# Kernel optimization log

Hardware: AMD Instinct MI355X
Metric: run time of the kernel (lower is better)

## Reference

```python
import jax, jax.numpy as jnp
import numpy as np

DIM = 1024
NUM_HEADS = 16
WINDOW_SIZE = 512
HEAD_DIM = DIM // NUM_HEADS
SCALE = HEAD_DIM ** (-0.5)


def setup_inputs() -> dict:
    key = jax.random.key(0)
    kq, kk, kv = jax.random.split(key, 3)
    shape = (2, NUM_HEADS, 2048, HEAD_DIM)
    q = jax.random.normal(kq, shape, dtype=jnp.float32)
    k = jax.random.normal(kk, shape, dtype=jnp.float32)
    v = jax.random.normal(kv, shape, dtype=jnp.float32)
    return {"q": q, "k": k, "v": v}


def reference(q, k, v):
    B, H, N, D = q.shape
    pos = jnp.arange(N)
    # causal + sliding window: col <= row and col >= row - w + 1
    window_mask = (pos[None, :] <= pos[:, None]) & (pos[None, :] >= pos[:, None] - WINDOW_SIZE + 1)  # (N, N)
    attn = jnp.einsum("bhnd,bhmd->bhnm", q, k) * SCALE  # (B, H, N, N)
    attn = jnp.where(window_mask[None, None], attn, -jnp.inf)
    attn = jax.nn.softmax(attn, axis=-1)
    attn = jnp.nan_to_num(attn, nan=0.0)
    return jnp.einsum("bhnm,bhmd->bhnd", attn, v)
```

## Files before the change

kernel.cpp:

```cpp
#include <hip/hip_runtime.h>
#include <math.h>


#define SEQ 2048
#define HD  64
#define BM  64
#define BN  64
#define LDR 72

typedef short short8 __attribute__((ext_vector_type(8)));
typedef float f32x4  __attribute__((ext_vector_type(4)));

static __device__ inline unsigned short f2bf(float f){
  union{float f; unsigned u;} un; un.f=f;
  return (unsigned short)((un.u + 0x7FFFu + ((un.u>>16)&1u))>>16);
}

__global__ __launch_bounds__(256) void swa_fwd(
    const float* __restrict__ q, const float* __restrict__ k,
    const float* __restrict__ v, float* __restrict__ out)
{
  __shared__ short Qs[BM*LDR];
  __shared__ short Ps[BM*LDR];
  __shared__ short Ks[2][BN*LDR];
  __shared__ short Vt[2][HD*LDR];

  const int tid=threadIdx.x, bid=blockIdx.x;
  const int mtile=bid&31, bh=bid>>5, m0=mtile*BM;
  const long base=(long)bh*SEQ*HD;
  const int wv=tid>>6, lane=tid&63, quad=lane>>4, l16=lane&15;
  const int dcol=lane;

  {
    const float4* qg=(const float4*)(q+base+(long)m0*HD);
    #pragma unroll
    for(int i=0;i<4;++i){
      int idx=i*256+tid, r=idx>>4, c4=idx&15;
      float4 f=qg[idx];
      ushort4 h; h.x=f2bf(f.x); h.y=f2bf(f.y); h.z=f2bf(f.z); h.w=f2bf(f.w);
      *(ushort4*)&Qs[r*LDR+c4*4]=h;
    }
  }

  const int tb=mtile, tlo=(tb>8)?(tb-8):0;

  float4 kreg[4];
  float  vcol[4][4];
  {
    const float4* kg=(const float4*)(k+base+(long)(tlo*BN)*HD);
    const float*  vg=v+base+(long)(tlo*BN)*HD;
    #pragma unroll
    for(int i=0;i<4;++i) kreg[i]=kg[i*256+tid];
    #pragma unroll
    for(int g=0;g<4;++g){
      int r0=wv*4+g*16;
      #pragma unroll
      for(int j=0;j<4;++j) vcol[g][j]=vg[(r0+j)*HD+dcol];
    }
  }
  __syncthreads();

  short8 qa[2];
  #pragma unroll
  for(int kk=0;kk<2;++kk)
    qa[kk]=*(const short8*)&Qs[(wv*16+l16)*LDR+kk*32+quad*8];

  {
    #pragma unroll
    for(int i=0;i<4;++i){
      int idx=i*256+tid, r=idx>>4, c4=idx&15;
      float4 fk=kreg[i];
      ushort4 hk; hk.x=f2bf(fk.x); hk.y=f2bf(fk.y); hk.z=f2bf(fk.z); hk.w=f2bf(fk.w);
      *(ushort4*)&Ks[0][r*LDR+c4*4]=hk;
    }
    #pragma unroll
    for(int g=0;g<4;++g){
      int r0=wv*4+g*16;
      ushort4 hv; hv.x=f2bf(vcol[g][0]); hv.y=f2bf(vcol[g][1]);
                  hv.z=f2bf(vcol[g][2]); hv.w=f2bf(vcol[g][3]);
      *(ushort4*)&Vt[0][dcol*LDR+r0]=hv;
    }
  }

  float lrun[4]={0.f,0.f,0.f,0.f};
  f32x4 oacc[4];
  #pragma unroll
  for(int dt=0;dt<4;++dt) oacc[dt]=(f32x4){0.f,0.f,0.f,0.f};

  __syncthreads();

  for(int t=tlo;t<=tb;++t){
    const int buf=(t-tlo)&1;
    const int j0=t*BN;

    f32x4 sacc[4];
    #pragma unroll
    for(int nt=0;nt<4;++nt) sacc[nt]=(f32x4){0.f,0.f,0.f,0.f};
    #pragma unroll
    for(int kk=0;kk<2;++kk){
      #pragma unroll
      for(int nt=0;nt<4;++nt){
        short8 kb=*(const short8*)&Ks[buf][(nt*16+l16)*LDR+kk*32+quad*8];
        sacc[nt]=__builtin_amdgcn_mfma_f32_16x16x32_bf16(qa[kk],kb,sacc[nt],0,0,0);
      }
    }

    if(t<tb){
      const float4* kg=(const float4*)(k+base+(long)((t+1)*BN)*HD);
      const float*  vg=v+base+(long)((t+1)*BN)*HD;
      #pragma unroll
      for(int i=0;i<4;++i) kreg[i]=kg[i*256+tid];
      #pragma unroll
      for(int g=0;g<4;++g){
        int r0=wv*4+g*16;
        #pragma unroll
        for(int j=0;j<4;++j) vcol[g][j]=vg[(r0+j)*HD+dcol];
      }
    }

    #pragma unroll
    for(int r=0;r<4;++r){
      const int grr=m0+wv*16+quad*4+r;
      #pragma unroll
      for(int nt=0;nt<4;++nt){
        const int gc=j0+nt*16+l16;
        float e=exp2f(sacc[nt][r]*0.18033688011112042f);
        float p=((gc<=grr)&&(gc>=grr-511))?e:0.f;
        lrun[r]+=p;
        Ps[(wv*16+quad*4+r)*LDR+nt*16+l16]=(short)f2bf(p);
      }
    }
    __syncthreads();

    #pragma unroll
    for(int kk=0;kk<2;++kk){
      short8 pa=*(const short8*)&Ps[(wv*16+l16)*LDR+kk*32+quad*8];
      #pragma unroll
      for(int dt=0;dt<4;++dt){
        short8 vb=*(const short8*)&Vt[buf][(dt*16+l16)*LDR+kk*32+quad*8];
        oacc[dt]=__builtin_amdgcn_mfma_f32_16x16x32_bf16(pa,vb,oacc[dt],0,0,0);
      }
    }

    if(t<tb){
      #pragma unroll
      for(int i=0;i<4;++i){
        int idx=i*256+tid, r=idx>>4, c4=idx&15;
        float4 fk=kreg[i];
        ushort4 hk; hk.x=f2bf(fk.x); hk.y=f2bf(fk.y); hk.z=f2bf(fk.z); hk.w=f2bf(fk.w);
        *(ushort4*)&Ks[buf^1][r*LDR+c4*4]=hk;
      }
      #pragma unroll
      for(int g=0;g<4;++g){
        int r0=wv*4+g*16;
        ushort4 hv; hv.x=f2bf(vcol[g][0]); hv.y=f2bf(vcol[g][1]);
                    hv.z=f2bf(vcol[g][2]); hv.w=f2bf(vcol[g][3]);
        *(ushort4*)&Vt[buf^1][dcol*LDR+r0]=hv;
      }
    }
    __syncthreads();
  }

  #pragma unroll
  for(int r=0;r<4;++r){
    float s=lrun[r];
    s+=__shfl_xor(s,1); s+=__shfl_xor(s,2); s+=__shfl_xor(s,4); s+=__shfl_xor(s,8);
    lrun[r]=(s>0.f)?(1.f/s):0.f;
  }
  #pragma unroll
  for(int r=0;r<4;++r){
    const int row=m0+wv*16+quad*4+r;
    #pragma unroll
    for(int dt=0;dt<4;++dt)
      out[base+(long)row*HD+dt*16+l16]=oacc[dt][r]*lrun[r];
  }
}

extern "C" void kernel_launch(void* const* d_in, const int* in_sizes, int n_in,
                              void* d_out, int out_size, void* d_ws, size_t ws_size,
                              hipStream_t stream) {
  const float* q=(const float*)d_in[0];
  const float* k=(const float*)d_in[1];
  const float* v=(const float*)d_in[2];
  float* o=(float*)d_out;
  dim3 grid(32*32);
  dim3 block(256);
  hipLaunchKernelGGL(swa_fwd, grid, block, 0, stream, q, k, v, o);
}
```

Measured before the change: 127.6 us.

## Pre-convert K/V to bf16 workspace and run LDS-free main attention kernel

```diff
diff --git a/kernel.cpp b/kernel.cpp
--- a/kernel.cpp
+++ b/kernel.cpp
@@ -5,7 +5,6 @@
 #define SEQ 2048
 #define HD  64
 #define BM  64
-#define BN  64
 #define LDR 72
 
 typedef short short8 __attribute__((ext_vector_type(8)));
@@ -14,6 +13,139 @@
 static __device__ inline unsigned short f2bf(float f){
   union{float f; unsigned u;} un; un.f=f;
   return (unsigned short)((un.u + 0x7FFFu + ((un.u>>16)&1u))>>16);
+}
+
+__global__ __launch_bounds__(256) void swa_prep(
+    const float* __restrict__ k, const float* __restrict__ v,
+    unsigned short* __restrict__ Kb, unsigned short* __restrict__ Vtb)
+{
+  __shared__ unsigned short Vs[64*68];
+  const int tid=threadIdx.x, bid=blockIdx.x;
+  const int kt=bid&31, bh=bid>>5;
+  const long tbase=(long)bh*SEQ*HD + (long)kt*64*HD;
+
+  #pragma unroll
+  for(int i=0;i<4;++i){
+    int idx=i*256+tid; int r=idx>>4, c4=idx&15;
+    float4 f=*(const float4*)(k + tbase + r*HD + c4*4);
+    ushort4 h; h.x=f2bf(f.x); h.y=f2bf(f.y); h.z=f2bf(f.z); h.w=f2bf(f.w);
+    *(ushort4*)(Kb + tbase + r*HD + c4*4) = h;
+  }
+  #pragma unroll
+  for(int i=0;i<4;++i){
+    int idx=i*256+tid; int r=idx>>4, c4=idx&15;
+    float4 f=*(const float4*)(v + tbase + r*HD + c4*4);
+    ushort4 h; h.x=f2bf(f.x); h.y=f2bf(f.y); h.z=f2bf(f.z); h.w=f2bf(f.w);
+    *(ushort4*)&Vs[r*68 + c4*4] = h;
+  }
+  __syncthreads();
+  const int d=tid>>2, c0=tid&3;
+  unsigned short tmp[16];
+  #pragma unroll
+  for(int e=0;e<16;++e) tmp[e]=Vs[(c0*16+e)*68 + d];
+  long vtoff=(long)bh*HD*SEQ + (long)d*SEQ + kt*64 + c0*16;
+  *(uint4*)(Vtb+vtoff)   = *(uint4*)&tmp[0];
+  *(uint4*)(Vtb+vtoff+8) = *(uint4*)&tmp[8];
+}
+
+__global__ __launch_bounds__(256) void swa_main(
+    const float* __restrict__ q,
+    const unsigned short* __restrict__ Kb,
+    const unsigned short* __restrict__ Vtb,
+    float* __restrict__ out)
+{
+  const int tid=threadIdx.x, bid=blockIdx.x;
+  const int mtile=bid&31, bh=bid>>5, m0=mtile*BM;
+  const long base=(long)bh*SEQ*HD;
+  const int wv=tid>>6, lane=tid&63, quad=lane>>4, l16=lane&15;
+
+  const int qrow = m0 + wv*16 + l16;
+  short8 qa[2];
+  {
+    const float* qp = q + base + (long)qrow*HD + quad*8;
+    const float C = 0.18033688011112042f;
+    #pragma unroll
+    for(int kk=0;kk<2;++kk){
+      float4 f0=*(const float4*)(qp+kk*32);
+      float4 f1=*(const float4*)(qp+kk*32+4);
+      short8 a;
+      a[0]=(short)f2bf(f0.x*C); a[1]=(short)f2bf(f0.y*C);
+      a[2]=(short)f2bf(f0.z*C); a[3]=(short)f2bf(f0.w*C);
+      a[4]=(short)f2bf(f1.x*C); a[5]=(short)f2bf(f1.y*C);
+      a[6]=(short)f2bf(f1.z*C); a[7]=(short)f2bf(f1.w*C);
+      qa[kk]=a;
+    }
+  }
+
+  const int rbase = 8*(l16>>2) + (l16&3);
+  const unsigned short* kp0 = Kb + (long)bh*SEQ*HD + (long)rbase*HD + quad*8;
+  const unsigned short* vp0 = Vtb + (long)bh*HD*SEQ + (long)l16*SEQ + quad*8;
+
+  f32x4 oacc[4];
+  #pragma unroll
+  for(int dt=0;dt<4;++dt) oacc[dt]=(f32x4){0.f,0.f,0.f,0.f};
+  float lrun=0.f;
+
+  const int tb=mtile, tlo=(mtile>=8)?(mtile-8):0;
+
+#define STEP(J0, MASKED)                                                        \
+  {                                                                             \
+    const int j0=(J0);                                                          \
+    f32x4 sacc[4];                                                              \
+    _Pragma("unroll") for(int nt=0;nt<4;++nt) sacc[nt]=(f32x4){0.f,0.f,0.f,0.f};\
+    _Pragma("unroll") for(int kk=0;kk<2;++kk){                                  \
+      _Pragma("unroll") for(int nt=0;nt<4;++nt){                                \
+        short8 ka = *(const short8*)(kp0 + (long)j0*HD                          \
+                       + (nt&1)*(4*HD) + (nt>>1)*(32*HD) + kk*32);              \
+        sacc[nt]=__builtin_amdgcn_mfma_f32_16x16x32_bf16(ka, qa[kk], sacc[nt],0,0,0); \
+      }                                                                         \
+    }                                                                           \
+    short8 vb[4][2];                                                            \
+    _Pragma("unroll") for(int dt=0;dt<4;++dt)                                   \
+      _Pragma("unroll") for(int kk=0;kk<2;++kk)                                 \
+        vb[dt][kk]=*(const short8*)(vp0 + (long)dt*16*SEQ + j0 + kk*32);        \
+    unsigned short pb[16];                                                      \
+    _Pragma("unroll") for(int nt=0;nt<4;++nt){                                  \
+      _Pragma("unroll") for(int r=0;r<4;++r){                                   \
+        float e=__builtin_amdgcn_exp2f(sacc[nt][r]);                            \
+        if (MASKED){                                                            \
+          int key=j0 + 8*quad + r + (nt&1)*4 + (nt>>1)*32;                      \
+          bool valid=(key<=qrow)&&(key+511>=qrow);                              \
+          e = valid ? e : 0.f;                                                  \
+        }                                                                       \
+        lrun += e;                                                              \
+        pb[nt*4+r]=f2bf(e);                                                     \
+      }                                                                         \
+    }                                                                           \
+    short8 pa0, pa1;                                                            \
+    _Pragma("unroll") for(int j=0;j<8;++j){ pa0[j]=(short)pb[j]; pa1[j]=(short)pb[8+j]; } \
+    _Pragma("unroll") for(int dt=0;dt<4;++dt){                                  \
+      oacc[dt]=__builtin_amdgcn_mfma_f32_16x16x32_bf16(pa0, vb[dt][0], oacc[dt],0,0,0); \
+      oacc[dt]=__builtin_amdgcn_mfma_f32_16x16x32_bf16(pa1, vb[dt][1], oacc[dt],0,0,0); \
+    }                                                                           \
+  }
+
+  if (mtile>=8){
+    STEP(tlo*BM, true);
+    for(int t=tlo+1;t<tb;++t) STEP(t*BM, false);
+    STEP(tb*BM, true);
+  } else {
+    for(int t=0;t<tb;++t) STEP(t*BM, false);
+    STEP(tb*BM, true);
+  }
+#undef STEP
+
+  lrun += __shfl_xor(lrun,16);
+  lrun += __shfl_xor(lrun,32);
+  float linv = 1.0f/lrun;
+  #pragma unroll
+  for(int r=0;r<4;++r){
+    float lr = __shfl(linv, quad*4+r);
+    const int orow = m0 + wv*16 + quad*4 + r;
+    #pragma unroll
+    for(int dt=0;dt<4;++dt)
+      out[base + (long)orow*HD + dt*16 + l16] = oacc[dt][r]*lr;
+  }
 }
 
 __global__ __launch_bounds__(256) void swa_fwd(
@@ -22,7 +154,7 @@
 {
   __shared__ short Qs[BM*LDR];
   __shared__ short Ps[BM*LDR];
-  __shared__ short Ks[2][BN*LDR];
+  __shared__ short Ks[2][BM*LDR];
   __shared__ short Vt[2][HD*LDR];
 
   const int tid=threadIdx.x, bid=blockIdx.x;
@@ -41,30 +173,23 @@
       *(ushort4*)&Qs[r*LDR+c4*4]=h;
     }
   }
-
   const int tb=mtile, tlo=(tb>8)?(tb-8):0;
-
-  float4 kreg[4];
-  float  vcol[4][4];
+  float4 kreg[4]; float vcol[4][4];
   {
-    const float4* kg=(const float4*)(k+base+(long)(tlo*BN)*HD);
-    const float*  vg=v+base+(long)(tlo*BN)*HD;
+    const float4* kg=(const float4*)(k+base+(long)(tlo*BM)*HD);
+    const float*  vg=v+base+(long)(tlo*BM)*HD;
     #pragma unroll
     for(int i=0;i<4;++i) kreg[i]=kg[i*256+tid];
     #pragma unroll
-    for(int g=0;g<4;++g){
-      int r0=wv*4+g*16;
-      #pragma unroll
-      for(int j=0;j<4;++j) vcol[g][j]=vg[(r0+j)*HD+dcol];
-    }
+    for(int g=0;g<4;++g){ int r0=wv*4+g*16;
+      #pragma unroll
+      for(int j=0;j<4;++j) vcol[g][j]=vg[(r0+j)*HD+dcol]; }
   }
   __syncthreads();
-
   short8 qa[2];
   #pragma unroll
   for(int kk=0;kk<2;++kk)
     qa[kk]=*(const short8*)&Qs[(wv*16+l16)*LDR+kk*32+quad*8];
-
   {
     #pragma unroll
     for(int i=0;i<4;++i){
@@ -74,25 +199,19 @@
       *(ushort4*)&Ks[0][r*LDR+c4*4]=hk;
     }
     #pragma unroll
-    for(int g=0;g<4;++g){
-      int r0=wv*4+g*16;
+    for(int g=0;g<4;++g){ int r0=wv*4+g*16;
       ushort4 hv; hv.x=f2bf(vcol[g][0]); hv.y=f2bf(vcol[g][1]);
                   hv.z=f2bf(vcol[g][2]); hv.w=f2bf(vcol[g][3]);
-      *(ushort4*)&Vt[0][dcol*LDR+r0]=hv;
-    }
-  }
-
+      *(ushort4*)&Vt[0][dcol*LDR+r0]=hv; }
+  }
   float lrun[4]={0.f,0.f,0.f,0.f};
   f32x4 oacc[4];
   #pragma unroll
   for(int dt=0;dt<4;++dt) oacc[dt]=(f32x4){0.f,0.f,0.f,0.f};
-
   __syncthreads();
 
   for(int t=tlo;t<=tb;++t){
-    const int buf=(t-tlo)&1;
-    const int j0=t*BN;
-
+    const int buf=(t-tlo)&1, j0=t*BM;
     f32x4 sacc[4];
     #pragma unroll
     for(int nt=0;nt<4;++nt) sacc[nt]=(f32x4){0.f,0.f,0.f,0.f};
@@ -104,20 +223,16 @@
         sacc[nt]=__builtin_amdgcn_mfma_f32_16x16x32_bf16(qa[kk],kb,sacc[nt],0,0,0);
       }
     }
-
     if(t<tb){
-      const float4* kg=(const float4*)(k+base+(long)((t+1)*BN)*HD);
-      const float*  vg=v+base+(long)((t+1)*BN)*HD;
+      const float4* kg=(const float4*)(k+base+(long)((t+1)*BM)*HD);
+      const float*  vg=v+base+(long)((t+1)*BM)*HD;
       #pragma unroll
       for(int i=0;i<4;++i) kreg[i]=kg[i*256+tid];
       #pragma unroll
-      for(int g=0;g<4;++g){
-        int r0=wv*4+g*16;
+      for(int g=0;g<4;++g){ int r0=wv*4+g*16;
         #pragma unroll
-        for(int j=0;j<4;++j) vcol[g][j]=vg[(r0+j)*HD+dcol];
-      }
-    }
-
+        for(int j=0;j<4;++j) vcol[g][j]=vg[(r0+j)*HD+dcol]; }
+    }
     #pragma unroll
     for(int r=0;r<4;++r){
       const int grr=m0+wv*16+quad*4+r;
@@ -131,7 +246,6 @@
       }
     }
     __syncthreads();
-
     #pragma unroll
     for(int kk=0;kk<2;++kk){
       short8 pa=*(const short8*)&Ps[(wv*16+l16)*LDR+kk*32+quad*8];
@@ -141,7 +255,6 @@
         oacc[dt]=__builtin_amdgcn_mfma_f32_16x16x32_bf16(pa,vb,oacc[dt],0,0,0);
       }
     }
-
     if(t<tb){
       #pragma unroll
       for(int i=0;i<4;++i){
@@ -151,16 +264,13 @@
         *(ushort4*)&Ks[buf^1][r*LDR+c4*4]=hk;
       }
       #pragma unroll
-      for(int g=0;g<4;++g){
-        int r0=wv*4+g*16;
+      for(int g=0;g<4;++g){ int r0=wv*4+g*16;
         ushort4 hv; hv.x=f2bf(vcol[g][0]); hv.y=f2bf(vcol[g][1]);
                     hv.z=f2bf(vcol[g][2]); hv.w=f2bf(vcol[g][3]);
-        *(ushort4*)&Vt[buf^1][dcol*LDR+r0]=hv;
-      }
+        *(ushort4*)&Vt[buf^1][dcol*LDR+r0]=hv; }
     }
     __syncthreads();
   }
-
   #pragma unroll
   for(int r=0;r<4;++r){
     float s=lrun[r];
@@ -183,7 +293,13 @@
   const float* k=(const float*)d_in[1];
   const float* v=(const float*)d_in[2];
   float* o=(float*)d_out;
-  dim3 grid(32*32);
-  dim3 block(256);
-  hipLaunchKernelGGL(swa_fwd, grid, block, 0, stream, q, k, v, o);
-}
+  const size_t NEED = 2ull * 32 * 2048 * 64 * 2;
+  if (ws_size >= NEED) {
+    unsigned short* Kb  = (unsigned short*)d_ws;
+    unsigned short* Vtb = Kb + 32ull*2048*64;
+    hipLaunchKernelGGL(swa_prep, dim3(1024), dim3(256), 0, stream, k, v, Kb, Vtb);
+    hipLaunchKernelGGL(swa_main, dim3(1024), dim3(256), 0, stream, q, Kb, Vtb, o);
+  } else {
+    hipLaunchKernelGGL(swa_fwd, dim3(1024), dim3(256), 0, stream, q, k, v, o);
+  }
+}
```

Result: slower. 174.3 us (+36.5%).
